# Kernel optimization log

Hardware: AMD Instinct MI355X
Metric: run time of the kernel (lower is better)

The kernel has to match this reference:

```python
import jax, jax.numpy as jnp
import numpy as np

B, S, H = 2, 2048, 2048
E, I, SH = 8, 768, 5632
TOP_K = 2


def setup_inputs() -> dict:
    key = jax.random.key(0)
    ks = jax.random.split(key, 8)
    sc = lambda *shape: 1.0 / np.sqrt(shape[-2] if len(shape) > 1 else 1.0)
    return {
        "hidden_states": jax.random.normal(ks[0], (B, S, H), jnp.float32),
        "router_w": jax.random.normal(ks[1], (H, E), jnp.float32) * (1.0 / np.sqrt(H)),
        "expert_gate_up_w": jax.random.normal(ks[2], (E, H, 2 * I), jnp.float32) * (1.0 / np.sqrt(H)),
        "expert_down_w": jax.random.normal(ks[3], (E, I, H), jnp.float32) * (1.0 / np.sqrt(I)),
        "shared_gate_w": jax.random.normal(ks[4], (H, SH), jnp.float32) * (1.0 / np.sqrt(H)),
        "shared_up_w": jax.random.normal(ks[5], (H, SH), jnp.float32) * (1.0 / np.sqrt(H)),
        "shared_down_w": jax.random.normal(ks[6], (SH, H), jnp.float32) * (1.0 / np.sqrt(SH)),
        "shared_expert_gate_w": jax.random.normal(ks[7], (H, 1), jnp.float32) * (1.0 / np.sqrt(H)),
    }


def reference(hidden_states, router_w, expert_gate_up_w, expert_down_w,
              shared_gate_w, shared_up_w, shared_down_w, shared_expert_gate_w):
    b, s, h = hidden_states.shape
    x = hidden_states.reshape(-1, h)  # [T, H]

    # Shared expert (SwiGLU) gated by sigmoid scalar gate per token.
    gate = jax.nn.silu((x @ shared_gate_w).astype(jnp.float32)).astype(x.dtype)
    shared_out = (gate * (x @ shared_up_w)) @ shared_down_w  # [T, H]
    shared_out = jax.nn.sigmoid(x @ shared_expert_gate_w) * shared_out

    # Router: softmax -> top-k -> renormalize -> dense routing weights [E, T].
    router_logits = x @ router_w  # [T, E]
    router_probs = jax.nn.softmax(router_logits, axis=-1)
    top_p, top_i = jax.lax.top_k(router_probs, TOP_K)  # [T, k]
    top_p = top_p / jnp.sum(top_p, axis=-1, keepdims=True)
    one_hot = jax.nn.one_hot(top_i, E, dtype=top_p.dtype)  # [T, k, E]
    routing_full = jnp.sum(one_hot * top_p[..., None], axis=1)  # [T, E]
    routing_full = routing_full.T.astype(x.dtype)  # [E, T]

    # Dense per-expert SwiGLU over all tokens (as in source einsums).
    gate_up = jnp.einsum('th,ehm->etm', x, expert_gate_up_w)  # [E, T, 2I]
    g, u = jnp.split(gate_up, 2, axis=-1)
    g = jax.nn.silu(g.astype(jnp.float32)).astype(x.dtype)
    expert_out = jnp.einsum('eti,eih->eth', u * g, expert_down_w)  # [E, T, H]

    expert_contribution = jnp.sum(expert_out * routing_full[:, :, None], axis=0)  # [T, H]
    out = (expert_contribution + shared_out).reshape(b, s, h)
    return out, router_logits
```

## Files before the change

### kernel.cpp

```cpp
#include <hip/hip_runtime.h>
#include <hip/hip_bf16.h>
#include <stdint.h>

#define DEVFN static __device__ __forceinline__

typedef __attribute__((ext_vector_type(8))) short bf16x8;
typedef __attribute__((ext_vector_type(4))) float f32x4;
typedef unsigned short u16;
typedef unsigned int u32;
typedef unsigned long long u64;

DEVFN u16 f2bf(float f) {
    union { float f; u32 u; } v; v.f = f;
    u32 r = v.u + 0x7FFFu + ((v.u >> 16) & 1u);
    return (u16)(r >> 16);
}

DEVFN void g2l16(const void* g, void* l) {
    __builtin_amdgcn_global_load_lds(
        (const __attribute__((address_space(1))) u32*)g,
        (__attribute__((address_space(3))) u32*)l, 16, 0, 0);
}

DEVFN void hbar() {
    __asm__ __volatile__("" ::: "memory");
    __builtin_amdgcn_s_barrier();
    __asm__ __volatile__("" ::: "memory");
}
DEVFN void vm4() { asm volatile("s_waitcnt vmcnt(4)" ::: "memory"); }
DEVFN void vm0() { asm volatile("s_waitcnt vmcnt(0)" ::: "memory"); }

#define MFMA16(a, b, c) __builtin_amdgcn_mfma_f32_16x16x32_bf16(a, b, c, 0, 0, 0)

__global__ __launch_bounds__(512, 2) void gemm8_swiglu_k(
    const u16* __restrict__ A, const u16* __restrict__ Bg,
    const u16* __restrict__ Bu, u16* __restrict__ out,
    int K, int nx, int ldc)
{
    extern __shared__ char smraw[];
    char* smA = smraw;
    char* smB = smraw + 65536;

    const int tid = threadIdx.x;
    const int lane = tid & 63, wv = tid >> 6;
    const int wm = wv >> 2, wn = wv & 3;
    const int l15 = lane & 15, kg = lane >> 4;

    const int nwg = gridDim.x;
    const int id = (blockIdx.x & 7) * (nwg >> 3) + (blockIdx.x >> 3);
    const int m0 = (id / nx) * 256, n0 = (id % nx) * 128;

    const u16* Ap  = A  + (long)m0 * K;
    const u16* Bgp = Bg + (long)n0 * K;
    const u16* Bup = Bu + (long)n0 * K;

    f32x4 accg[8][2], accu[8][2];
#pragma unroll
    for (int i = 0; i < 8; ++i)
#pragma unroll
        for (int j = 0; j < 2; ++j) {
            accg[i][j] = f32x4{0.f, 0.f, 0.f, 0.f};
            accu[i][j] = f32x4{0.f, 0.f, 0.f, 0.f};
        }

    auto stA = [&](int kt, int hh, int buf) {
        const u16* src = Ap + ((long)hh * 128) * K + kt * 64;
        char* dst = smA + buf * 32768 + hh * 16384;
#pragma unroll
        for (int i = 0; i < 2; ++i) {
            int slot = i * 512 + tid;
            int row = slot >> 3, ch = slot & 7;
            g2l16(src + (long)row * K + ((ch ^ (row & 7)) << 3), dst + slot * 16);
        }
    };
    auto stB = [&](int kt, int hh, int buf) {
        const u16* src = (hh ? Bup : Bgp) + kt * 64;
        char* dst = smB + buf * 32768 + hh * 16384;
#pragma unroll
        for (int i = 0; i < 2; ++i) {
            int slot = i * 512 + tid;
            int row = slot >> 3, ch = slot & 7;
            g2l16(src + (long)row * K + ((ch ^ (row & 7)) << 3), dst + slot * 16);
        }
    };
    auto frag = [&](const char* base, int r, int c) -> bf16x8 {
        return *(const __attribute__((address_space(3))) bf16x8*)
            (base + r * 128 + (((c) ^ (r & 7)) << 4));
    };

    stA(0, 0, 0); stA(0, 1, 0);
    stB(0, 0, 0); stB(0, 1, 0);
    stB(1, 0, 1); stB(1, 1, 1);
    vm4();
    hbar();

    const int nk = K >> 6;
    for (int kt = 0; kt < nk; kt += 2) {
        const bool more = (kt + 2) < nk;
#pragma unroll
        for (int h = 0; h < 2; ++h) {
            const char* ab = smA + h * 32768;
            const char* bb = smB + h * 32768;
            bf16x8 bgv[2][2], buv[2][2];
#pragma unroll
            for (int p = 0; p < 4; ++p) {
                if (p == 0) {
#pragma unroll
                    for (int fn = 0; fn < 2; ++fn)
#pragma unroll
                        for (int s = 0; s < 2; ++s) {
                            int rB = wn * 32 + fn * 16 + l15;
                            bgv[fn][s] = frag(bb, rB, s * 4 + kg);
                            buv[fn][s] = frag(bb + 16384, rB, s * 4 + kg);
                        }
                }
                bf16x8 av[2][2];
#pragma unroll
                for (int am = 0; am < 2; ++am)
#pragma unroll
                    for (int s = 0; s < 2; ++s)
                        av[am][s] = frag(ab, wm * 128 + (p * 2 + am) * 16 + l15,
                                         s * 4 + kg);
                if (h == 0) {
                    if (p == 0)      { stA(kt + 1, 0, 1); stA(kt + 1, 1, 1); }
                    else if (p == 1) { if (more) stB(kt + 2, 0, 0); }
                    else if (p == 2) { if (more) stB(kt + 2, 1, 0); }
                    else             { if (more) vm4(); else vm0(); }
                } else {
                    if (more) {
                        if (p == 0)      stA(kt + 2, 0, 0);
                        else if (p == 1) stA(kt + 2, 1, 0);
                        else if (p == 2) stB(kt + 3, 0, 1);
                        else             { stB(kt + 3, 1, 1); vm4(); }
                    }
                }
                hbar();
                __builtin_amdgcn_sched_barrier(0);
                __builtin_amdgcn_s_setprio(1);
#pragma unroll
                for (int am = 0; am < 2; ++am)
#pragma unroll
                    for (int s = 0; s < 2; ++s)
#pragma unroll
                        for (int fn = 0; fn < 2; ++fn) {
                            accg[p * 2 + am][fn] = MFMA16(av[am][s], bgv[fn][s],
                                                          accg[p * 2 + am][fn]);
                            accu[p * 2 + am][fn] = MFMA16(av[am][s], buv[fn][s],
                                                          accu[p * 2 + am][fn]);
                        }
                __builtin_amdgcn_s_setprio(0);
                __builtin_amdgcn_sched_barrier(0);
                hbar();
            }
        }
    }

    const int lq = lane >> 4;
#pragma unroll
    for (int fm = 0; fm < 8; ++fm)
#pragma unroll
        for (int j = 0; j < 4; ++j) {
            int row = m0 + wm * 128 + fm * 16 + lq * 4 + j;
#pragma unroll
            for (int fn = 0; fn < 2; ++fn) {
                int col = n0 + wn * 32 + fn * 16 + l15;
                float g = accg[fm][fn][j], u = accu[fm][fn][j];
                float s = g * (1.f / (1.f + __expf(-g))) * u;
                out[(long)row * ldc + col] = f2bf(s);
            }
        }
}

__global__ __launch_bounds__(512, 2) void gemm8e_swiglu_k(
    const u16* __restrict__ xb, const u16* __restrict__ Beg,
    const u16* __restrict__ Beu, const int* __restrict__ tok,
    const int* __restrict__ cntp, u16* __restrict__ eact,
    int K, int ldc, int cap)
{
    const int e = blockIdx.z;
    const int m0 = blockIdx.y * 256;
    if (m0 >= cntp[e]) return;
    const int n0 = blockIdx.x * 128;

    extern __shared__ char smraw[];
    char* smA = smraw;
    char* smB = smraw + 65536;

    const int tid = threadIdx.x;
    const int lane = tid & 63, wv = tid >> 6;
    const int wm = wv >> 2, wn = wv & 3;
    const int l15 = lane & 15, kg = lane >> 4;

    const int r0 = tid >> 3, ch = tid & 7;
    const int swz = (ch ^ (r0 & 7)) << 3;
    const int* tseg = tok + (long)e * cap + m0;
    const u16* pa00 = xb + (long)tseg[r0] * K + swz;
    const u16* pa01 = xb + (long)tseg[64 + r0] * K + swz;
    const u16* pa10 = xb + (long)tseg[128 + r0] * K + swz;
    const u16* pa11 = xb + (long)tseg[192 + r0] * K + swz;

    const u16* Bgp = Beg + ((long)e * ldc + n0) * K;
    const u16* Bup = Beu + ((long)e * ldc + n0) * K;

    f32x4 accg[8][2], accu[8][2];
#pragma unroll
    for (int i = 0; i < 8; ++i)
#pragma unroll
        for (int j = 0; j < 2; ++j) {
            accg[i][j] = f32x4{0.f, 0.f, 0.f, 0.f};
            accu[i][j] = f32x4{0.f, 0.f, 0.f, 0.f};
        }

    auto stA = [&](int kt, int hh, int buf) {
        char* dst = smA + buf * 32768 + hh * 16384;
        const u16* p0 = hh ? pa10 : pa00;
        const u16* p1 = hh ? pa11 : pa01;
        g2l16(p0 + kt * 64, dst + (long)tid * 16);
        g2l16(p1 + kt * 64, dst + (long)(512 + tid) * 16);
    };
    auto stB = [&](int kt, int hh, int buf) {
        const u16* src = (hh ? Bup : Bgp) + kt * 64;
        char* dst = smB + buf * 32768 + hh * 16384;
#pragma unroll
        for (int i = 0; i < 2; ++i) {
            int slot = i * 512 + tid;
            int row = slot >> 3, c = slot & 7;
            g2l16(src + (long)row * K + ((c ^ (row & 7)) << 3), dst + slot * 16);
        }
    };
    auto frag = [&](const char* base, int r, int c) -> bf16x8 {
        return *(const __attribute__((address_space(3))) bf16x8*)
            (base + r * 128 + (((c) ^ (r & 7)) << 4));
    };

    stA(0, 0, 0); stA(0, 1, 0);
    stB(0, 0, 0); stB(0, 1, 0);
    stB(1, 0, 1); stB(1, 1, 1);
    vm4();
    hbar();

    const int nk = K >> 6;
    for (int kt = 0; kt < nk; kt += 2) {
        const bool more = (kt + 2) < nk;
#pragma unroll
        for (int h = 0; h < 2; ++h) {
            const char* ab = smA + h * 32768;
            const char* bb = smB + h * 32768;
            bf16x8 bgv[2][2], buv[2][2];
#pragma unroll
            for (int p = 0; p < 4; ++p) {
                if (p == 0) {
#pragma unroll
                    for (int fn = 0; fn < 2; ++fn)
#pragma unroll
                        for (int s = 0; s < 2; ++s) {
                            int rB = wn * 32 + fn * 16 + l15;
                            bgv[fn][s] = frag(bb, rB, s * 4 + kg);
                            buv[fn][s] = frag(bb + 16384, rB, s * 4 + kg);
                        }
                }
                bf16x8 av[2][2];
#pragma unroll
                for (int am = 0; am < 2; ++am)
#pragma unroll
                    for (int s = 0; s < 2; ++s)
                        av[am][s] = frag(ab, wm * 128 + (p * 2 + am) * 16 + l15,
                                         s * 4 + kg);
                if (h == 0) {
                    if (p == 0)      { stA(kt + 1, 0, 1); stA(kt + 1, 1, 1); }
                    else if (p == 1) { if (more) stB(kt + 2, 0, 0); }
                    else if (p == 2) { if (more) stB(kt + 2, 1, 0); }
                    else             { if (more) vm4(); else vm0(); }
                } else {
                    if (more) {
                        if (p == 0)      stA(kt + 2, 0, 0);
                        else if (p == 1) stA(kt + 2, 1, 0);
                        else if (p == 2) stB(kt + 3, 0, 1);
                        else             { stB(kt + 3, 1, 1); vm4(); }
                    }
                }
                hbar();
                __builtin_amdgcn_sched_barrier(0);
                __builtin_amdgcn_s_setprio(1);
#pragma unroll
                for (int am = 0; am < 2; ++am)
#pragma unroll
                    for (int s = 0; s < 2; ++s)
#pragma unroll
                        for (int fn = 0; fn < 2; ++fn) {
                            accg[p * 2 + am][fn] = MFMA16(av[am][s], bgv[fn][s],
                                                          accg[p * 2 + am][fn]);
                            accu[p * 2 + am][fn] = MFMA16(av[am][s], buv[fn][s],
                                                          accu[p * 2 + am][fn]);
                        }
                __builtin_amdgcn_s_setprio(0);
                __builtin_amdgcn_sched_barrier(0);
                hbar();
            }
        }
    }

    const int lq = lane >> 4;
#pragma unroll
    for (int fm = 0; fm < 8; ++fm)
#pragma unroll
        for (int j = 0; j < 4; ++j) {
            long row = (long)e * cap + m0 + wm * 128 + fm * 16 + lq * 4 + j;
#pragma unroll
            for (int fn = 0; fn < 2; ++fn) {
                int col = n0 + wn * 32 + fn * 16 + l15;
                float g = accg[fm][fn][j], u = accu[fm][fn][j];
                float s = g * (1.f / (1.f + __expf(-g))) * u;
                eact[row * ldc + col] = f2bf(s);
            }
        }
}

template<int NSLOT>
DEVFN void stage(const u16* __restrict__ src, int ldk, u16* lds, int tid) {
#pragma unroll
    for (int i = 0; i < NSLOT / 256; ++i) {
        int slot = i * 256 + tid;
        int row = slot >> 2, chunk = slot & 3;
        int kg = chunk ^ ((row >> 1) & 3);
        g2l16(src + (long)row * ldk + kg * 8, lds + slot * 8);
    }
}

DEVFN bf16x8 ld_frag(const u16* lds, int row, int kg) {
    int chunk = kg ^ ((row >> 1) & 3);
    const u16* p = lds + row * 32 + chunk * 8;
    return *(const __attribute__((address_space(3))) bf16x8*)p;
}

__global__ __launch_bounds__(256) void gemm_down_k(
    const u16* __restrict__ A, const u16* __restrict__ B,
    float* __restrict__ C, const float* __restrict__ gvec,
    int K, int ldc)
{
    __shared__ u16 sm[2][8192];
    const int tid = threadIdx.x;
    const int lane = tid & 63, wv = tid >> 6;
    const int wm = wv >> 1, wn = wv & 1;
    const int m0 = blockIdx.y * 128, n0 = blockIdx.x * 128;
    const u16* Ab = A + (long)m0 * K;
    const u16* Bb = B + (long)n0 * K;

    f32x4 acc[4][4];
#pragma unroll
    for (int i = 0; i < 4; ++i)
#pragma unroll
        for (int j = 0; j < 4; ++j) acc[i][j] = f32x4{0.f, 0.f, 0.f, 0.f};

    stage<512>(Ab, K, &sm[0][0], tid);
    stage<512>(Bb, K, &sm[0][4096], tid);

    const int nk = K >> 5;
    for (int kt = 0; kt < nk; ++kt) {
        const int cur = kt & 1;
        __syncthreads();
        if (kt + 1 < nk) {
            stage<512>(Ab + (kt + 1) * 32, K, &sm[cur ^ 1][0], tid);
            stage<512>(Bb + (kt + 1) * 32, K, &sm[cur ^ 1][4096], tid);
        }
        const int l15 = lane & 15, kg = lane >> 4;
        bf16x8 av[4], bv[4];
#pragma unroll
        for (int f = 0; f < 4; ++f) {
            av[f] = ld_frag(&sm[cur][0],    wm * 64 + f * 16 + l15, kg);
            bv[f] = ld_frag(&sm[cur][4096], wn * 64 + f * 16 + l15, kg);
        }
#pragma unroll
        for (int fm = 0; fm < 4; ++fm)
#pragma unroll
            for (int fn = 0; fn < 4; ++fn)
                acc[fm][fn] = MFMA16(av[fm], bv[fn], acc[fm][fn]);
    }

    const int l15 = lane & 15, lq = lane >> 4;
#pragma unroll
    for (int fm = 0; fm < 4; ++fm) {
#pragma unroll
        for (int j = 0; j < 4; ++j) {
            int row = m0 + wm * 64 + fm * 16 + lq * 4 + j;
            float gmul = gvec[row];
#pragma unroll
            for (int fn = 0; fn < 4; ++fn) {
                int col = n0 + wn * 64 + fn * 16 + l15;
                C[(long)row * ldc + col] = acc[fm][fn][j] * gmul;
            }
        }
    }
}

__global__ __launch_bounds__(256) void gemm_down_moe_k(
    const u16* __restrict__ eact, const u16* __restrict__ Bed,
    float* __restrict__ out, const int* __restrict__ tok,
    const float* __restrict__ wrow, const int* __restrict__ cntp,
    int K, int ldc, int cap)
{
    const int e = blockIdx.z;
    const int m0 = blockIdx.y * 128;
    if (m0 >= cntp[e]) return;
    const int n0 = blockIdx.x * 128;

    __shared__ u16 sm[2][8192];
    const int tid = threadIdx.x;
    const int lane = tid & 63, wv = tid >> 6;
    const int wm = wv >> 1, wn = wv & 1;
    const u16* Ab = eact + ((long)e * cap + m0) * K;
    const u16* Bb = Bed + (long)e * ldc * K + (long)n0 * K;

    f32x4 acc[4][4];
#pragma unroll
    for (int i = 0; i < 4; ++i)
#pragma unroll
        for (int j = 0; j < 4; ++j) acc[i][j] = f32x4{0.f, 0.f, 0.f, 0.f};

    stage<512>(Ab, K, &sm[0][0], tid);
    stage<512>(Bb, K, &sm[0][4096], tid);

    const int nk = K >> 5;
    for (int kt = 0; kt < nk; ++kt) {
        const int cur = kt & 1;
        __syncthreads();
        if (kt + 1 < nk) {
            stage<512>(Ab + (kt + 1) * 32, K, &sm[cur ^ 1][0], tid);
            stage<512>(Bb + (kt + 1) * 32, K, &sm[cur ^ 1][4096], tid);
        }
        const int l15 = lane & 15, kg = lane >> 4;
        bf16x8 av[4], bv[4];
#pragma unroll
        for (int f = 0; f < 4; ++f) {
            av[f] = ld_frag(&sm[cur][0],    wm * 64 + f * 16 + l15, kg);
            bv[f] = ld_frag(&sm[cur][4096], wn * 64 + f * 16 + l15, kg);
        }
#pragma unroll
        for (int fm = 0; fm < 4; ++fm)
#pragma unroll
            for (int fn = 0; fn < 4; ++fn)
                acc[fm][fn] = MFMA16(av[fm], bv[fn], acc[fm][fn]);
    }

    const int l15 = lane & 15, lq = lane >> 4;
#pragma unroll
    for (int fm = 0; fm < 4; ++fm) {
#pragma unroll
        for (int j = 0; j < 4; ++j) {
            long crow = (long)e * cap + m0 + wm * 64 + fm * 16 + lq * 4 + j;
            float w = wrow[crow];
            if (w != 0.f) {
                long t = tok[crow];
#pragma unroll
                for (int fn = 0; fn < 4; ++fn) {
                    int col = n0 + wn * 64 + fn * 16 + l15;
                    atomicAdd(out + t * ldc + col, acc[fm][fn][j] * w);
                }
            }
        }
    }
}

__global__ __launch_bounds__(256) void router_k(
    const float* __restrict__ x, const float* __restrict__ rw,
    const float* __restrict__ sgw, float* __restrict__ logits,
    int2* __restrict__ te, float2* __restrict__ tw,
    float* __restrict__ sig, int T, int H)
{
    const int tid = threadIdx.x, lane = tid & 63, wv = tid >> 6;
    const int t = blockIdx.x * 4 + wv;
    const float* xr = x + (long)t * H;
    float acc[8] = {0, 0, 0, 0, 0, 0, 0, 0};
    float as = 0.f;
    for (int h = lane; h < H; h += 64) {
        float xv = xr[h];
        const float* r = rw + h * 8;
#pragma unroll
        for (int e = 0; e < 8; ++e) acc[e] += xv * r[e];
        as += xv * sgw[h];
    }
#pragma unroll
    for (int off = 32; off; off >>= 1) {
#pragma unroll
        for (int e = 0; e < 8; ++e) acc[e] += __shfl_xor(acc[e], off);
        as += __shfl_xor(as, off);
    }
    if (lane == 0) {
        float mx = acc[0];
#pragma unroll
        for (int e = 1; e < 8; ++e) mx = fmaxf(mx, acc[e]);
        float p[8], sum = 0.f;
#pragma unroll
        for (int e = 0; e < 8; ++e) { p[e] = expf(acc[e] - mx); sum += p[e]; }
        int i1 = 0;
#pragma unroll
        for (int e = 1; e < 8; ++e) if (p[e] > p[i1]) i1 = e;
        int i2 = (i1 == 0) ? 1 : 0;
#pragma unroll
        for (int e = 0; e < 8; ++e) if (e != i1 && p[e] > p[i2]) i2 = e;
        float den = p[i1] + p[i2];
        te[t] = make_int2(i1, i2);
        tw[t] = make_float2(p[i1] / den, p[i2] / den);
#pragma unroll
        for (int e = 0; e < 8; ++e) logits[(long)t * 8 + e] = acc[e];
        sig[t] = 1.f / (1.f + expf(-as));
    }
}

__global__ __launch_bounds__(256) void compact_k(
    const int2* __restrict__ te, const float2* __restrict__ tw,
    int* __restrict__ tok, float* __restrict__ wrow,
    int* __restrict__ cntp, int T, int cap)
{
    const int e = blockIdx.x;
    const int tid = threadIdx.x, lane = tid & 63, wv = tid >> 6;
    __shared__ int wtot[4];
    int cnt = 0;
    for (int c0 = 0; c0 < T; c0 += 256) {
        int t = c0 + tid;
        int2 ids = te[t];
        float2 ws = tw[t];
        float w = (ids.x == e) ? ws.x : ((ids.y == e) ? ws.y : -1.f);
        bool sel = (w >= 0.f);
        u64 b = __ballot(sel);
        int rln = __popcll(b & ((1ull << lane) - 1ull));
        if (lane == 0) wtot[wv] = __popcll(b);
        __syncthreads();
        int rank = rln, tot = 0;
#pragma unroll
        for (int k = 0; k < 4; ++k) { if (k < wv) rank += wtot[k]; tot += wtot[k]; }
        if (sel) {
            int pos = cnt + rank;
            if (pos < cap) {
                tok[(long)e * cap + pos] = t;
                wrow[(long)e * cap + pos] = w;
            }
        }
        cnt += tot;
        __syncthreads();
    }
    if (cnt > cap) cnt = cap;
    int cp = (cnt + 255) & ~255;
    if (cp > cap) cp = cap;
    for (int p = cnt + tid; p < cp; p += 256) {
        tok[(long)e * cap + p] = 0;
        wrow[(long)e * cap + p] = 0.f;
    }
    if (tid == 0) cntp[e] = cp;
}

__global__ __launch_bounds__(256) void transpose_k(
    const float* __restrict__ src0, long src_zstr, int src_ld,
    u16* __restrict__ dst0, long dst_zstr, int dst_ld)
{
    __shared__ float tile[32][33];
    const float* src = src0 + (long)blockIdx.z * src_zstr;
    u16* dst = dst0 + (long)blockIdx.z * dst_zstr;
    int r0 = blockIdx.y * 32, c0 = blockIdx.x * 32;
    int tx = threadIdx.x, ty = threadIdx.y;
#pragma unroll
    for (int k = 0; k < 4; ++k)
        tile[ty + 8 * k][tx] = src[(long)(r0 + ty + 8 * k) * src_ld + c0 + tx];
    __syncthreads();
#pragma unroll
    for (int k = 0; k < 4; ++k)
        dst[(long)(c0 + ty + 8 * k) * dst_ld + r0 + tx] = f2bf(tile[tx][ty + 8 * k]);
}

__global__ __launch_bounds__(256) void cvt_x_k(const float* __restrict__ x,
                                               u16* __restrict__ xb)
{
    long i = ((long)blockIdx.x * 256 + threadIdx.x) * 4;
    float4 v = *(const float4*)(x + i);
    union { u16 s[4]; uint2 v2; } o;
    o.s[0] = f2bf(v.x); o.s[1] = f2bf(v.y); o.s[2] = f2bf(v.z); o.s[3] = f2bf(v.w);
    *(uint2*)(xb + i) = o.v2;
}

extern "C" void kernel_launch(void* const* d_in, const int* in_sizes, int n_in,
                              void* d_out, int out_size, void* d_ws, size_t ws_size,
                              hipStream_t stream) {
    (void)in_sizes; (void)n_in; (void)out_size; (void)ws_size;
    const int Hd = 2048, E = 8, I = 768, SH = 5632, T = 4096, CAP = 2048;

    const float* x    = (const float*)d_in[0];
    const float* rw   = (const float*)d_in[1];
    const float* egu  = (const float*)d_in[2];
    const float* edw  = (const float*)d_in[3];
    const float* sgw  = (const float*)d_in[4];
    const float* suw  = (const float*)d_in[5];
    const float* sdw  = (const float*)d_in[6];
    const float* segw = (const float*)d_in[7];
    float* out = (float*)d_out;
    float* logits = out + (size_t)T * Hd;

    char* wsp = (char*)d_ws;
    size_t off = 0;
    auto alloc = [&](size_t bytes) {
        void* p = wsp + off; off += (bytes + 255) & ~(size_t)255; return p;
    };
    u16* xb   = (u16*)alloc((size_t)T * Hd * 2);
    u16* Bgs  = (u16*)alloc((size_t)SH * Hd * 2);
    u16* Bus  = (u16*)alloc((size_t)SH * Hd * 2);
    u16* Bds  = (u16*)alloc((size_t)Hd * SH * 2);
    u16* Beg  = (u16*)alloc((size_t)E * I * Hd * 2);
    u16* Beu  = (u16*)alloc((size_t)E * I * Hd * 2);
    u16* Bed  = (u16*)alloc((size_t)E * Hd * I * 2);
    u16* hs   = (u16*)alloc((size_t)T * SH * 2);
    u16* eact = (u16*)alloc((size_t)E * CAP * I * 2);
    int2*   te   = (int2*)alloc((size_t)T * 8);
    float2* tw   = (float2*)alloc((size_t)T * 8);
    int*    tok  = (int*)alloc((size_t)E * CAP * 4);
    float*  wrow = (float*)alloc((size_t)E * CAP * 4);
    int*    cntp = (int*)alloc(64);
    float*  sig  = (float*)alloc((size_t)T * 4);

    hipFuncSetAttribute((const void*)gemm8_swiglu_k,
                        hipFuncAttributeMaxDynamicSharedMemorySize, 131072);
    hipFuncSetAttribute((const void*)gemm8e_swiglu_k,
                        hipFuncAttributeMaxDynamicSharedMemorySize, 131072);

    dim3 tb(32, 8);
    cvt_x_k<<<(T * Hd) / 1024, 256, 0, stream>>>(x, xb);
    router_k<<<T / 4, 256, 0, stream>>>(x, rw, segw, logits, te, tw, sig, T, Hd);
    compact_k<<<E, 256, 0, stream>>>(te, tw, tok, wrow, cntp, T, CAP);

    transpose_k<<<dim3(SH / 32, Hd / 32), tb, 0, stream>>>(sgw, 0, SH, Bgs, 0, Hd);
    transpose_k<<<dim3(SH / 32, Hd / 32), tb, 0, stream>>>(suw, 0, SH, Bus, 0, Hd);
    transpose_k<<<dim3(Hd / 32, SH / 32), tb, 0, stream>>>(sdw, 0, Hd, Bds, 0, SH);
    transpose_k<<<dim3(I / 32, Hd / 32, E), tb, 0, stream>>>(
        egu, (long)Hd * 2 * I, 2 * I, Beg, (long)I * Hd, Hd);
    transpose_k<<<dim3(I / 32, Hd / 32, E), tb, 0, stream>>>(
        egu + I, (long)Hd * 2 * I, 2 * I, Beu, (long)I * Hd, Hd);
    transpose_k<<<dim3(Hd / 32, I / 32, E), tb, 0, stream>>>(
        edw, (long)I * Hd, Hd, Bed, (long)Hd * I, I);

    gemm8_swiglu_k<<<dim3((SH / 128) * (T / 256)), 512, 131072, stream>>>(
        xb, Bgs, Bus, hs, Hd, SH / 128, SH);
    gemm_down_k<<<dim3(Hd / 128, T / 128), 256, 0, stream>>>(
        hs, Bds, out, sig, SH, Hd);
    gemm8e_swiglu_k<<<dim3(I / 128, CAP / 256, E), 512, 131072, stream>>>(
        xb, Beg, Beu, tok, cntp, eact, Hd, I, CAP);
    gemm_down_moe_k<<<dim3(Hd / 128, CAP / 128, E), 256, 0, stream>>>(
        eact, Bed, out, tok, wrow, cntp, I, Hd, CAP);
}
```

Measured before the change: 578.6 us.

## Port down-projection GEMMs to 256x256 pipelined kernel with split-K and atomics

Replaces the simple 128x128 double-buffered down-projection kernels (shared and MoE) with the 512-thread 256x256 tile pipeline already used by the gate/up kernels, now wrapped in a shared macro. The shared down GEMM is split along K into two halves that accumulate into a zeroed output with atomics. The B fragments for the next half are also prefetched one phase early to hide LDS latency. This aims to raise MFMA utilisation and data reuse in the down GEMMs, at the cost of an extra memset and atomic traffic on the output.

```diff
diff --git a/kernel.cpp b/kernel.cpp
--- a/kernel.cpp
+++ b/kernel.cpp
@@ -32,6 +32,81 @@
 
 #define MFMA16(a, b, c) __builtin_amdgcn_mfma_f32_16x16x32_bf16(a, b, c, 0, 0, 0)
 
+#define FR(base, r, c) \
+    (*(const __attribute__((address_space(3))) bf16x8*) \
+        ((base) + (r) * 128 + ((((c)) ^ ((r) & 7)) << 4)))
+
+#define RDB8(h) { \
+    const char* _b0 = smB + (h) * 32768; \
+    bgv[h][0][0] = FR(_b0,         wn * 32 +  0 + l15, 0 + kg); \
+    bgv[h][0][1] = FR(_b0,         wn * 32 +  0 + l15, 4 + kg); \
+    bgv[h][1][0] = FR(_b0,         wn * 32 + 16 + l15, 0 + kg); \
+    bgv[h][1][1] = FR(_b0,         wn * 32 + 16 + l15, 4 + kg); \
+    buv[h][0][0] = FR(_b0 + 16384, wn * 32 +  0 + l15, 0 + kg); \
+    buv[h][0][1] = FR(_b0 + 16384, wn * 32 +  0 + l15, 4 + kg); \
+    buv[h][1][0] = FR(_b0 + 16384, wn * 32 + 16 + l15, 0 + kg); \
+    buv[h][1][1] = FR(_b0 + 16384, wn * 32 + 16 + l15, 4 + kg); }
+
+#define PH(h, p, ...) { \
+    const char* _a = smA + (h) * 32768; \
+    bf16x8 a0s0 = FR(_a, wm * 128 + ((p) * 2 + 0) * 16 + l15, 0 + kg); \
+    bf16x8 a0s1 = FR(_a, wm * 128 + ((p) * 2 + 0) * 16 + l15, 4 + kg); \
+    bf16x8 a1s0 = FR(_a, wm * 128 + ((p) * 2 + 1) * 16 + l15, 0 + kg); \
+    bf16x8 a1s1 = FR(_a, wm * 128 + ((p) * 2 + 1) * 16 + l15, 4 + kg); \
+    __VA_ARGS__ \
+    hbar(); \
+    __builtin_amdgcn_sched_barrier(0); \
+    __builtin_amdgcn_s_setprio(1); \
+    accg[(p)*2+0][0] = MFMA16(a0s0, bgv[h][0][0], accg[(p)*2+0][0]); \
+    accu[(p)*2+0][0] = MFMA16(a0s0, buv[h][0][0], accu[(p)*2+0][0]); \
+    accg[(p)*2+0][1] = MFMA16(a0s0, bgv[h][1][0], accg[(p)*2+0][1]); \
+    accu[(p)*2+0][1] = MFMA16(a0s0, buv[h][1][0], accu[(p)*2+0][1]); \
+    accg[(p)*2+0][0] = MFMA16(a0s1, bgv[h][0][1], accg[(p)*2+0][0]); \
+    accu[(p)*2+0][0] = MFMA16(a0s1, buv[h][0][1], accu[(p)*2+0][0]); \
+    accg[(p)*2+0][1] = MFMA16(a0s1, bgv[h][1][1], accg[(p)*2+0][1]); \
+    accu[(p)*2+0][1] = MFMA16(a0s1, buv[h][1][1], accu[(p)*2+0][1]); \
+    accg[(p)*2+1][0] = MFMA16(a1s0, bgv[h][0][0], accg[(p)*2+1][0]); \
+    accu[(p)*2+1][0] = MFMA16(a1s0, buv[h][0][0], accu[(p)*2+1][0]); \
+    accg[(p)*2+1][1] = MFMA16(a1s0, bgv[h][1][0], accg[(p)*2+1][1]); \
+    accu[(p)*2+1][1] = MFMA16(a1s0, buv[h][1][0], accu[(p)*2+1][1]); \
+    accg[(p)*2+1][0] = MFMA16(a1s1, bgv[h][0][1], accg[(p)*2+1][0]); \
+    accu[(p)*2+1][0] = MFMA16(a1s1, buv[h][0][1], accu[(p)*2+1][0]); \
+    accg[(p)*2+1][1] = MFMA16(a1s1, bgv[h][1][1], accg[(p)*2+1][1]); \
+    accu[(p)*2+1][1] = MFMA16(a1s1, buv[h][1][1], accu[(p)*2+1][1]); \
+    __builtin_amdgcn_s_setprio(0); \
+    __builtin_amdgcn_sched_barrier(0); \
+    hbar(); }
+
+#define KLOOP(nk) \
+    stA(0, 0, 0); stA(0, 1, 0); \
+    stB(0, 0, 0); stB(0, 1, 0); \
+    stB(1, 0, 1); stB(1, 1, 1); \
+    vm4(); \
+    hbar(); \
+    RDB8(0); \
+    for (int kt = 0; kt < (nk); kt += 2) { \
+        const bool more = (kt + 2) < (nk); \
+        PH(0, 0, stA(kt + 1, 0, 1); stA(kt + 1, 1, 1); ) \
+        PH(0, 1, if (more) stB(kt + 2, 0, 0); ) \
+        PH(0, 2, if (more) stB(kt + 2, 1, 0); ) \
+        PH(0, 3, if (more) vm4(); else vm0(); RDB8(1); ) \
+        PH(1, 0, if (more) stA(kt + 2, 0, 0); ) \
+        PH(1, 1, if (more) stA(kt + 2, 1, 0); ) \
+        PH(1, 2, if (more) stB(kt + 3, 0, 1); ) \
+        PH(1, 3, if (more) { stB(kt + 3, 1, 1); vm4(); RDB8(0); } ) \
+    }
+
+#define ACC_DECL \
+    f32x4 accg[8][2], accu[8][2]; \
+    _Pragma("unroll") \
+    for (int i = 0; i < 8; ++i) \
+        _Pragma("unroll") \
+        for (int j = 0; j < 2; ++j) { \
+            accg[i][j] = f32x4{0.f, 0.f, 0.f, 0.f}; \
+            accu[i][j] = f32x4{0.f, 0.f, 0.f, 0.f}; \
+        } \
+    bf16x8 bgv[2][2][2], buv[2][2][2];
+
 __global__ __launch_bounds__(512, 2) void gemm8_swiglu_k(
     const u16* __restrict__ A, const u16* __restrict__ Bg,
     const u16* __restrict__ Bu, u16* __restrict__ out,
@@ -54,14 +129,7 @@
     const u16* Bgp = Bg + (long)n0 * K;
     const u16* Bup = Bu + (long)n0 * K;
 
-    f32x4 accg[8][2], accu[8][2];
-#pragma unroll
-    for (int i = 0; i < 8; ++i)
-#pragma unroll
-        for (int j = 0; j < 2; ++j) {
-            accg[i][j] = f32x4{0.f, 0.f, 0.f, 0.f};
-            accu[i][j] = f32x4{0.f, 0.f, 0.f, 0.f};
-        }
+    ACC_DECL;
 
     auto stA = [&](int kt, int hh, int buf) {
         const u16* src = Ap + ((long)hh * 128) * K + kt * 64;
@@ -83,77 +151,8 @@
             g2l16(src + (long)row * K + ((ch ^ (row & 7)) << 3), dst + slot * 16);
         }
     };
-    auto frag = [&](const char* base, int r, int c) -> bf16x8 {
-        return *(const __attribute__((address_space(3))) bf16x8*)
-            (base + r * 128 + (((c) ^ (r & 7)) << 4));
-    };
-
-    stA(0, 0, 0); stA(0, 1, 0);
-    stB(0, 0, 0); stB(0, 1, 0);
-    stB(1, 0, 1); stB(1, 1, 1);
-    vm4();
-    hbar();
-
-    const int nk = K >> 6;
-    for (int kt = 0; kt < nk; kt += 2) {
-        const bool more = (kt + 2) < nk;
-#pragma unroll
-        for (int h = 0; h < 2; ++h) {
-            const char* ab = smA + h * 32768;
-            const char* bb = smB + h * 32768;
-            bf16x8 bgv[2][2], buv[2][2];
-#pragma unroll
-            for (int p = 0; p < 4; ++p) {
-                if (p == 0) {
-#pragma unroll
-                    for (int fn = 0; fn < 2; ++fn)
-#pragma unroll
-                        for (int s = 0; s < 2; ++s) {
-                            int rB = wn * 32 + fn * 16 + l15;
-                            bgv[fn][s] = frag(bb, rB, s * 4 + kg);
-                            buv[fn][s] = frag(bb + 16384, rB, s * 4 + kg);
-                        }
-                }
-                bf16x8 av[2][2];
-#pragma unroll
-                for (int am = 0; am < 2; ++am)
-#pragma unroll
-                    for (int s = 0; s < 2; ++s)
-                        av[am][s] = frag(ab, wm * 128 + (p * 2 + am) * 16 + l15,
-                                         s * 4 + kg);
-                if (h == 0) {
-                    if (p == 0)      { stA(kt + 1, 0, 1); stA(kt + 1, 1, 1); }
-                    else if (p == 1) { if (more) stB(kt + 2, 0, 0); }
-                    else if (p == 2) { if (more) stB(kt + 2, 1, 0); }
-                    else             { if (more) vm4(); else vm0(); }
-                } else {
-                    if (more) {
-                        if (p == 0)      stA(kt + 2, 0, 0);
-                        else if (p == 1) stA(kt + 2, 1, 0);
-                        else if (p == 2) stB(kt + 3, 0, 1);
-                        else             { stB(kt + 3, 1, 1); vm4(); }
-                    }
-                }
-                hbar();
-                __builtin_amdgcn_sched_barrier(0);
-                __builtin_amdgcn_s_setprio(1);
-#pragma unroll
-                for (int am = 0; am < 2; ++am)
-#pragma unroll
-                    for (int s = 0; s < 2; ++s)
-#pragma unroll
-                        for (int fn = 0; fn < 2; ++fn) {
-                            accg[p * 2 + am][fn] = MFMA16(av[am][s], bgv[fn][s],
-                                                          accg[p * 2 + am][fn]);
-                            accu[p * 2 + am][fn] = MFMA16(av[am][s], buv[fn][s],
-                                                          accu[p * 2 + am][fn]);
-                        }
-                __builtin_amdgcn_s_setprio(0);
-                __builtin_amdgcn_sched_barrier(0);
-                hbar();
-            }
-        }
-    }
+
+    KLOOP(K >> 6);
 
     const int lq = lane >> 4;
 #pragma unroll
@@ -202,14 +201,7 @@
     const u16* Bgp = Beg + ((long)e * ldc + n0) * K;
     const u16* Bup = Beu + ((long)e * ldc + n0) * K;
 
-    f32x4 accg[8][2], accu[8][2];
-#pragma unroll
-    for (int i = 0; i < 8; ++i)
-#pragma unroll
-        for (int j = 0; j < 2; ++j) {
-            accg[i][j] = f32x4{0.f, 0.f, 0.f, 0.f};
-            accu[i][j] = f32x4{0.f, 0.f, 0.f, 0.f};
-        }
+    ACC_DECL;
 
     auto stA = [&](int kt, int hh, int buf) {
         char* dst = smA + buf * 32768 + hh * 16384;
@@ -228,77 +220,8 @@
             g2l16(src + (long)row * K + ((c ^ (row & 7)) << 3), dst + slot * 16);
         }
     };
-    auto frag = [&](const char* base, int r, int c) -> bf16x8 {
-        return *(const __attribute__((address_space(3))) bf16x8*)
-            (base + r * 128 + (((c) ^ (r & 7)) << 4));
-    };
-
-    stA(0, 0, 0); stA(0, 1, 0);
-    stB(0, 0, 0); stB(0, 1, 0);
-    stB(1, 0, 1); stB(1, 1, 1);
-    vm4();
-    hbar();
-
-    const int nk = K >> 6;
-    for (int kt = 0; kt < nk; kt += 2) {
-        const bool more = (kt + 2) < nk;
-#pragma unroll
-        for (int h = 0; h < 2; ++h) {
-            const char* ab = smA + h * 32768;
-            const char* bb = smB + h * 32768;
-            bf16x8 bgv[2][2], buv[2][2];
-#pragma unroll
-            for (int p = 0; p < 4; ++p) {
-                if (p == 0) {
-#pragma unroll
-                    for (int fn = 0; fn < 2; ++fn)
-#pragma unroll
-                        for (int s = 0; s < 2; ++s) {
-                            int rB = wn * 32 + fn * 16 + l15;
-                            bgv[fn][s] = frag(bb, rB, s * 4 + kg);
-                            buv[fn][s] = frag(bb + 16384, rB, s * 4 + kg);
-                        }
-                }
-                bf16x8 av[2][2];
-#pragma unroll
-                for (int am = 0; am < 2; ++am)
-#pragma unroll
-                    for (int s = 0; s < 2; ++s)
-                        av[am][s] = frag(ab, wm * 128 + (p * 2 + am) * 16 + l15,
-                                         s * 4 + kg);
-                if (h == 0) {
-                    if (p == 0)      { stA(kt + 1, 0, 1); stA(kt + 1, 1, 1); }
-                    else if (p == 1) { if (more) stB(kt + 2, 0, 0); }
-                    else if (p == 2) { if (more) stB(kt + 2, 1, 0); }
-                    else             { if (more) vm4(); else vm0(); }
-                } else {
-                    if (more) {
-                        if (p == 0)      stA(kt + 2, 0, 0);
-                        else if (p == 1) stA(kt + 2, 1, 0);
-                        else if (p == 2) stB(kt + 3, 0, 1);
-                        else             { stB(kt + 3, 1, 1); vm4(); }
-                    }
-                }
-                hbar();
-                __builtin_amdgcn_sched_barrier(0);
-                __builtin_amdgcn_s_setprio(1);
-#pragma unroll
-                for (int am = 0; am < 2; ++am)
-#pragma unroll
-                    for (int s = 0; s < 2; ++s)
-#pragma unroll
-                        for (int fn = 0; fn < 2; ++fn) {
-                            accg[p * 2 + am][fn] = MFMA16(av[am][s], bgv[fn][s],
-                                                          accg[p * 2 + am][fn]);
-                            accu[p * 2 + am][fn] = MFMA16(av[am][s], buv[fn][s],
-                                                          accu[p * 2 + am][fn]);
-                        }
-                __builtin_amdgcn_s_setprio(0);
-                __builtin_amdgcn_sched_barrier(0);
-                hbar();
-            }
-        }
-    }
+
+    KLOOP(K >> 6);
 
     const int lq = lane >> 4;
 #pragma unroll
@@ -316,149 +239,134 @@
         }
 }
 
-template<int NSLOT>
-DEVFN void stage(const u16* __restrict__ src, int ldk, u16* lds, int tid) {
-#pragma unroll
-    for (int i = 0; i < NSLOT / 256; ++i) {
-        int slot = i * 256 + tid;
-        int row = slot >> 2, chunk = slot & 3;
-        int kg = chunk ^ ((row >> 1) & 3);
-        g2l16(src + (long)row * ldk + kg * 8, lds + slot * 8);
-    }
-}
-
-DEVFN bf16x8 ld_frag(const u16* lds, int row, int kg) {
-    int chunk = kg ^ ((row >> 1) & 3);
-    const u16* p = lds + row * 32 + chunk * 8;
-    return *(const __attribute__((address_space(3))) bf16x8*)p;
-}
-
-__global__ __launch_bounds__(256) void gemm_down_k(
+__global__ __launch_bounds__(512, 2) void gemm8_downks_k(
     const u16* __restrict__ A, const u16* __restrict__ B,
-    float* __restrict__ C, const float* __restrict__ gvec,
-    int K, int ldc)
-{
-    __shared__ u16 sm[2][8192];
+    float* __restrict__ out, const float* __restrict__ sig,
+    int K, int nkh, int ldc)
+{
+    extern __shared__ char smraw[];
+    char* smA = smraw;
+    char* smB = smraw + 65536;
+
     const int tid = threadIdx.x;
     const int lane = tid & 63, wv = tid >> 6;
-    const int wm = wv >> 1, wn = wv & 1;
-    const int m0 = blockIdx.y * 128, n0 = blockIdx.x * 128;
-    const u16* Ab = A + (long)m0 * K;
-    const u16* Bb = B + (long)n0 * K;
-
-    f32x4 acc[4][4];
-#pragma unroll
-    for (int i = 0; i < 4; ++i)
-#pragma unroll
-        for (int j = 0; j < 4; ++j) acc[i][j] = f32x4{0.f, 0.f, 0.f, 0.f};
-
-    stage<512>(Ab, K, &sm[0][0], tid);
-    stage<512>(Bb, K, &sm[0][4096], tid);
-
-    const int nk = K >> 5;
-    for (int kt = 0; kt < nk; ++kt) {
-        const int cur = kt & 1;
-        __syncthreads();
-        if (kt + 1 < nk) {
-            stage<512>(Ab + (kt + 1) * 32, K, &sm[cur ^ 1][0], tid);
-            stage<512>(Bb + (kt + 1) * 32, K, &sm[cur ^ 1][4096], tid);
-        }
-        const int l15 = lane & 15, kg = lane >> 4;
-        bf16x8 av[4], bv[4];
-#pragma unroll
-        for (int f = 0; f < 4; ++f) {
-            av[f] = ld_frag(&sm[cur][0],    wm * 64 + f * 16 + l15, kg);
-            bv[f] = ld_frag(&sm[cur][4096], wn * 64 + f * 16 + l15, kg);
-        }
-#pragma unroll
-        for (int fm = 0; fm < 4; ++fm)
-#pragma unroll
-            for (int fn = 0; fn < 4; ++fn)
-                acc[fm][fn] = MFMA16(av[fm], bv[fn], acc[fm][fn]);
-    }
-
-    const int l15 = lane & 15, lq = lane >> 4;
-#pragma unroll
-    for (int fm = 0; fm < 4; ++fm) {
+    const int wm = wv >> 2, wn = wv & 3;
+    const int l15 = lane & 15, kg = lane >> 4;
+
+    const int m0 = blockIdx.y * 256, n0 = blockIdx.x * 256;
+    const long k0 = (long)blockIdx.z * nkh * 64;
+
+    const u16* Ap  = A + (long)m0 * K + k0;
+    const u16* Blo = B + ((long)(n0      ) * K) + k0;
+    const u16* Bhi = B + ((long)(n0 + 128) * K) + k0;
+
+    ACC_DECL;
+
+    auto stA = [&](int kt, int hh, int buf) {
+        const u16* src = Ap + ((long)hh * 128) * K + kt * 64;
+        char* dst = smA + buf * 32768 + hh * 16384;
+#pragma unroll
+        for (int i = 0; i < 2; ++i) {
+            int slot = i * 512 + tid;
+            int row = slot >> 3, ch = slot & 7;
+            g2l16(src + (long)row * K + ((ch ^ (row & 7)) << 3), dst + slot * 16);
+        }
+    };
+    auto stB = [&](int kt, int hh, int buf) {
+        const u16* src = (hh ? Bhi : Blo) + kt * 64;
+        char* dst = smB + buf * 32768 + hh * 16384;
+#pragma unroll
+        for (int i = 0; i < 2; ++i) {
+            int slot = i * 512 + tid;
+            int row = slot >> 3, ch = slot & 7;
+            g2l16(src + (long)row * K + ((ch ^ (row & 7)) << 3), dst + slot * 16);
+        }
+    };
+
+    KLOOP(nkh);
+
+    const int lq = lane >> 4;
+#pragma unroll
+    for (int fm = 0; fm < 8; ++fm)
 #pragma unroll
         for (int j = 0; j < 4; ++j) {
-            int row = m0 + wm * 64 + fm * 16 + lq * 4 + j;
-            float gmul = gvec[row];
-#pragma unroll
-            for (int fn = 0; fn < 4; ++fn) {
-                int col = n0 + wn * 64 + fn * 16 + l15;
-                C[(long)row * ldc + col] = acc[fm][fn][j] * gmul;
+            int row = m0 + wm * 128 + fm * 16 + lq * 4 + j;
+            float s = sig[row];
+#pragma unroll
+            for (int fn = 0; fn < 2; ++fn) {
+                int col = n0 + wn * 32 + fn * 16 + l15;
+                atomicAdd(out + (long)row * ldc + col, accg[fm][fn][j] * s);
+                atomicAdd(out + (long)row * ldc + col + 128, accu[fm][fn][j] * s);
             }
         }
-    }
-}
-
-__global__ __launch_bounds__(256) void gemm_down_moe_k(
+}
+
+__global__ __launch_bounds__(512, 2) void gemm8_edown_k(
     const u16* __restrict__ eact, const u16* __restrict__ Bed,
     float* __restrict__ out, const int* __restrict__ tok,
     const float* __restrict__ wrow, const int* __restrict__ cntp,
-    int K, int ldc, int cap)
+    int K, int Hd, int cap)
 {
     const int e = blockIdx.z;
-    const int m0 = blockIdx.y * 128;
+    const int m0 = blockIdx.y * 256;
     if (m0 >= cntp[e]) return;
-    const int n0 = blockIdx.x * 128;
-
-    __shared__ u16 sm[2][8192];
+    const int n0 = blockIdx.x * 256;
+
+    extern __shared__ char smraw[];
+    char* smA = smraw;
+    char* smB = smraw + 65536;
+
     const int tid = threadIdx.x;
     const int lane = tid & 63, wv = tid >> 6;
-    const int wm = wv >> 1, wn = wv & 1;
-    const u16* Ab = eact + ((long)e * cap + m0) * K;
-    const u16* Bb = Bed + (long)e * ldc * K + (long)n0 * K;
-
-    f32x4 acc[4][4];
-#pragma unroll
-    for (int i = 0; i < 4; ++i)
-#pragma unroll
-        for (int j = 0; j < 4; ++j) acc[i][j] = f32x4{0.f, 0.f, 0.f, 0.f};
-
-    stage<512>(Ab, K, &sm[0][0], tid);
-    stage<512>(Bb, K, &sm[0][4096], tid);
-
-    const int nk = K >> 5;
-    for (int kt = 0; kt < nk; ++kt) {
-        const int cur = kt & 1;
-        __syncthreads();
-        if (kt + 1 < nk) {
-            stage<512>(Ab + (kt + 1) * 32, K, &sm[cur ^ 1][0], tid);
-            stage<512>(Bb + (kt + 1) * 32, K, &sm[cur ^ 1][4096], tid);
-        }
-        const int l15 = lane & 15, kg = lane >> 4;
-        bf16x8 av[4], bv[4];
-#pragma unroll
-        for (int f = 0; f < 4; ++f) {
-            av[f] = ld_frag(&sm[cur][0],    wm * 64 + f * 16 + l15, kg);
-            bv[f] = ld_frag(&sm[cur][4096], wn * 64 + f * 16 + l15, kg);
-        }
-#pragma unroll
-        for (int fm = 0; fm < 4; ++fm)
-#pragma unroll
-            for (int fn = 0; fn < 4; ++fn)
-                acc[fm][fn] = MFMA16(av[fm], bv[fn], acc[fm][fn]);
-    }
-
-    const int l15 = lane & 15, lq = lane >> 4;
-#pragma unroll
-    for (int fm = 0; fm < 4; ++fm) {
+    const int wm = wv >> 2, wn = wv & 3;
+    const int l15 = lane & 15, kg = lane >> 4;
+
+    const u16* Ap  = eact + ((long)e * cap + m0) * K;
+    const u16* Blo = Bed + ((long)e * Hd + n0      ) * K;
+    const u16* Bhi = Bed + ((long)e * Hd + n0 + 128) * K;
+
+    ACC_DECL;
+
+    auto stA = [&](int kt, int hh, int buf) {
+        const u16* src = Ap + ((long)hh * 128) * K + kt * 64;
+        char* dst = smA + buf * 32768 + hh * 16384;
+#pragma unroll
+        for (int i = 0; i < 2; ++i) {
+            int slot = i * 512 + tid;
+            int row = slot >> 3, ch = slot & 7;
+            g2l16(src + (long)row * K + ((ch ^ (row & 7)) << 3), dst + slot * 16);
+        }
+    };
+    auto stB = [&](int kt, int hh, int buf) {
+        const u16* src = (hh ? Bhi : Blo) + kt * 64;
+        char* dst = smB + buf * 32768 + hh * 16384;
+#pragma unroll
+        for (int i = 0; i < 2; ++i) {
+            int slot = i * 512 + tid;
+            int row = slot >> 3, ch = slot & 7;
+            g2l16(src + (long)row * K + ((ch ^ (row & 7)) << 3), dst + slot * 16);
+        }
+    };
+
+    KLOOP(K >> 6);
+
+    const int lq = lane >> 4;
+#pragma unroll
+    for (int fm = 0; fm < 8; ++fm)
 #pragma unroll
         for (int j = 0; j < 4; ++j) {
-            long crow = (long)e * cap + m0 + wm * 64 + fm * 16 + lq * 4 + j;
+            long crow = (long)e * cap + m0 + wm * 128 + fm * 16 + lq * 4 + j;
             float w = wrow[crow];
             if (w != 0.f) {
                 long t = tok[crow];
 #pragma unroll
-                for (int fn = 0; fn < 4; ++fn) {
-                    int col = n0 + wn * 64 + fn * 16 + l15;
-                    atomicAdd(out + t * ldc + col, acc[fm][fn][j] * w);
+                for (int fn = 0; fn < 2; ++fn) {
+                    int col = n0 + wn * 32 + fn * 16 + l15;
+                    atomicAdd(out + t * Hd + col, accg[fm][fn][j] * w);
+                    atomicAdd(out + t * Hd + col + 128, accu[fm][fn][j] * w);
                 }
             }
         }
-    }
 }
 
 __global__ __launch_bounds__(256) void router_k(
@@ -619,8 +527,13 @@
                         hipFuncAttributeMaxDynamicSharedMemorySize, 131072);
     hipFuncSetAttribute((const void*)gemm8e_swiglu_k,
                         hipFuncAttributeMaxDynamicSharedMemorySize, 131072);
+    hipFuncSetAttribute((const void*)gemm8_downks_k,
+                        hipFuncAttributeMaxDynamicSharedMemorySize, 131072);
+    hipFuncSetAttribute((const void*)gemm8_edown_k,
+                        hipFuncAttributeMaxDynamicSharedMemorySize, 131072);
 
     dim3 tb(32, 8);
+    hipMemsetAsync(out, 0, (size_t)T * Hd * 4, stream);
     cvt_x_k<<<(T * Hd) / 1024, 256, 0, stream>>>(x, xb);
     router_k<<<T / 4, 256, 0, stream>>>(x, rw, segw, logits, te, tw, sig, T, Hd);
     compact_k<<<E, 256, 0, stream>>>(te, tw, tok, wrow, cntp, T, CAP);
@@ -637,10 +550,10 @@
 
     gemm8_swiglu_k<<<dim3((SH / 128) * (T / 256)), 512, 131072, stream>>>(
         xb, Bgs, Bus, hs, Hd, SH / 128, SH);
-    gemm_down_k<<<dim3(Hd / 128, T / 128), 256, 0, stream>>>(
-        hs, Bds, out, sig, SH, Hd);
+    gemm8_downks_k<<<dim3(Hd / 256, T / 256, 2), 512, 131072, stream>>>(
+        hs, Bds, out, sig, SH, (SH / 64) / 2, Hd);
     gemm8e_swiglu_k<<<dim3(I / 128, CAP / 256, E), 512, 131072, stream>>>(
         xb, Beg, Beu, tok, cntp, eact, Hd, I, CAP);
-    gemm_down_moe_k<<<dim3(Hd / 128, CAP / 128, E), 256, 0, stream>>>(
+    gemm8_edown_k<<<dim3(Hd / 256, CAP / 256, E), 512, 131072, stream>>>(
         eact, Bed, out, tok, wrow, cntp, I, Hd, CAP);
 }
```

Result: slower. 805.1 us (+39.1%).

## Replace shared-expert down GEMM with 256x256 split-K pipelined kernel using atomics

Applied to the files above, without the earlier changes.

The simple 128x128 double-buffered shared-expert down-projection GEMM is replaced with a 512-thread kernel that reuses the 8-wave, 256x256-tile pipelined structure of the gate/up kernel. K is split in two across blockIdx.z, and partial results are combined with float atomicAdd into a zeroed output, so a memset is added before the launches. The goal is higher MFMA utilisation, more data reuse per tile, and enough blocks to fill the GPU (16x8x2). The cost is atomic traffic, a non-deterministic summation order, and an extra memset.

```diff
diff --git a/kernel.cpp b/kernel.cpp
--- a/kernel.cpp
+++ b/kernel.cpp
@@ -316,6 +316,144 @@
         }
 }
 
+__global__ __launch_bounds__(512, 2) void gemm8_downks_k(
+    const u16* __restrict__ A, const u16* __restrict__ B,
+    float* __restrict__ out, const float* __restrict__ sig,
+    int K, int nkh, int ldc)
+{
+    extern __shared__ char smraw[];
+    char* smA = smraw;
+    char* smB = smraw + 65536;
+
+    const int tid = threadIdx.x;
+    const int lane = tid & 63, wv = tid >> 6;
+    const int wm = wv >> 2, wn = wv & 3;
+    const int l15 = lane & 15, kg = lane >> 4;
+
+    const int m0 = blockIdx.y * 256, n0 = blockIdx.x * 256;
+    const long k0 = (long)blockIdx.z * nkh * 64;
+
+    const u16* Ap  = A + (long)m0 * K + k0;
+    const u16* Blo = B + (long)n0 * K + k0;
+    const u16* Bhi = B + (long)(n0 + 128) * K + k0;
+
+    f32x4 accg[8][2], accu[8][2];
+#pragma unroll
+    for (int i = 0; i < 8; ++i)
+#pragma unroll
+        for (int j = 0; j < 2; ++j) {
+            accg[i][j] = f32x4{0.f, 0.f, 0.f, 0.f};
+            accu[i][j] = f32x4{0.f, 0.f, 0.f, 0.f};
+        }
+
+    auto stA = [&](int kt, int hh, int buf) {
+        const u16* src = Ap + ((long)hh * 128) * K + kt * 64;
+        char* dst = smA + buf * 32768 + hh * 16384;
+#pragma unroll
+        for (int i = 0; i < 2; ++i) {
+            int slot = i * 512 + tid;
+            int row = slot >> 3, ch = slot & 7;
+            g2l16(src + (long)row * K + ((ch ^ (row & 7)) << 3), dst + slot * 16);
+        }
+    };
+    auto stB = [&](int kt, int hh, int buf) {
+        const u16* src = (hh ? Bhi : Blo) + kt * 64;
+        char* dst = smB + buf * 32768 + hh * 16384;
+#pragma unroll
+        for (int i = 0; i < 2; ++i) {
+            int slot = i * 512 + tid;
+            int row = slot >> 3, ch = slot & 7;
+            g2l16(src + (long)row * K + ((ch ^ (row & 7)) << 3), dst + slot * 16);
+        }
+    };
+    auto frag = [&](const char* base, int r, int c) -> bf16x8 {
+        return *(const __attribute__((address_space(3))) bf16x8*)
+            (base + r * 128 + (((c) ^ (r & 7)) << 4));
+    };
+
+    stA(0, 0, 0); stA(0, 1, 0);
+    stB(0, 0, 0); stB(0, 1, 0);
+    stB(1, 0, 1); stB(1, 1, 1);
+    vm4();
+    hbar();
+
+    const int nk = nkh;
+    for (int kt = 0; kt < nk; kt += 2) {
+        const bool more = (kt + 2) < nk;
+#pragma unroll
+        for (int h = 0; h < 2; ++h) {
+            const char* ab = smA + h * 32768;
+            const char* bb = smB + h * 32768;
+            bf16x8 bgv[2][2], buv[2][2];
+#pragma unroll
+            for (int p = 0; p < 4; ++p) {
+                if (p == 0) {
+#pragma unroll
+                    for (int fn = 0; fn < 2; ++fn)
+#pragma unroll
+                        for (int s = 0; s < 2; ++s) {
+                            int rB = wn * 32 + fn * 16 + l15;
+                            bgv[fn][s] = frag(bb, rB, s * 4 + kg);
+                            buv[fn][s] = frag(bb + 16384, rB, s * 4 + kg);
+                        }
+                }
+                bf16x8 av[2][2];
+#pragma unroll
+                for (int am = 0; am < 2; ++am)
+#pragma unroll
+                    for (int s = 0; s < 2; ++s)
+                        av[am][s] = frag(ab, wm * 128 + (p * 2 + am) * 16 + l15,
+                                         s * 4 + kg);
+                if (h == 0) {
+                    if (p == 0)      { stA(kt + 1, 0, 1); stA(kt + 1, 1, 1); }
+                    else if (p == 1) { if (more) stB(kt + 2, 0, 0); }
+                    else if (p == 2) { if (more) stB(kt + 2, 1, 0); }
+                    else             { if (more) vm4(); else vm0(); }
+                } else {
+                    if (more) {
+                        if (p == 0)      stA(kt + 2, 0, 0);
+                        else if (p == 1) stA(kt + 2, 1, 0);
+                        else if (p == 2) stB(kt + 3, 0, 1);
+                        else             { stB(kt + 3, 1, 1); vm4(); }
+                    }
+                }
+                hbar();
+                __builtin_amdgcn_sched_barrier(0);
+                __builtin_amdgcn_s_setprio(1);
+#pragma unroll
+                for (int am = 0; am < 2; ++am)
+#pragma unroll
+                    for (int s = 0; s < 2; ++s)
+#pragma unroll
+                        for (int fn = 0; fn < 2; ++fn) {
+                            accg[p * 2 + am][fn] = MFMA16(av[am][s], bgv[fn][s],
+                                                          accg[p * 2 + am][fn]);
+                            accu[p * 2 + am][fn] = MFMA16(av[am][s], buv[fn][s],
+                                                          accu[p * 2 + am][fn]);
+                        }
+                __builtin_amdgcn_s_setprio(0);
+                __builtin_amdgcn_sched_barrier(0);
+                hbar();
+            }
+        }
+    }
+
+    const int lq = lane >> 4;
+#pragma unroll
+    for (int fm = 0; fm < 8; ++fm)
+#pragma unroll
+        for (int j = 0; j < 4; ++j) {
+            int row = m0 + wm * 128 + fm * 16 + lq * 4 + j;
+            float s = sig[row];
+#pragma unroll
+            for (int fn = 0; fn < 2; ++fn) {
+                int col = n0 + wn * 32 + fn * 16 + l15;
+                atomicAdd(out + (long)row * ldc + col, accg[fm][fn][j] * s);
+                atomicAdd(out + (long)row * ldc + col + 128, accu[fm][fn][j] * s);
+            }
+        }
+}
+
 template<int NSLOT>
 DEVFN void stage(const u16* __restrict__ src, int ldk, u16* lds, int tid) {
 #pragma unroll
@@ -331,66 +469,6 @@
     int chunk = kg ^ ((row >> 1) & 3);
     const u16* p = lds + row * 32 + chunk * 8;
     return *(const __attribute__((address_space(3))) bf16x8*)p;
-}
-
-__global__ __launch_bounds__(256) void gemm_down_k(
-    const u16* __restrict__ A, const u16* __restrict__ B,
-    float* __restrict__ C, const float* __restrict__ gvec,
-    int K, int ldc)
-{
-    __shared__ u16 sm[2][8192];
-    const int tid = threadIdx.x;
-    const int lane = tid & 63, wv = tid >> 6;
-    const int wm = wv >> 1, wn = wv & 1;
-    const int m0 = blockIdx.y * 128, n0 = blockIdx.x * 128;
-    const u16* Ab = A + (long)m0 * K;
-    const u16* Bb = B + (long)n0 * K;
-
-    f32x4 acc[4][4];
-#pragma unroll
-    for (int i = 0; i < 4; ++i)
-#pragma unroll
-        for (int j = 0; j < 4; ++j) acc[i][j] = f32x4{0.f, 0.f, 0.f, 0.f};
-
-    stage<512>(Ab, K, &sm[0][0], tid);
-    stage<512>(Bb, K, &sm[0][4096], tid);
-
-    const int nk = K >> 5;
-    for (int kt = 0; kt < nk; ++kt) {
-        const int cur = kt & 1;
-        __syncthreads();
-        if (kt + 1 < nk) {
-            stage<512>(Ab + (kt + 1) * 32, K, &sm[cur ^ 1][0], tid);
-            stage<512>(Bb + (kt + 1) * 32, K, &sm[cur ^ 1][4096], tid);
-        }
-        const int l15 = lane & 15, kg = lane >> 4;
-        bf16x8 av[4], bv[4];
-#pragma unroll
-        for (int f = 0; f < 4; ++f) {
-            av[f] = ld_frag(&sm[cur][0],    wm * 64 + f * 16 + l15, kg);
-            bv[f] = ld_frag(&sm[cur][4096], wn * 64 + f * 16 + l15, kg);
-        }
-#pragma unroll
-        for (int fm = 0; fm < 4; ++fm)
-#pragma unroll
-            for (int fn = 0; fn < 4; ++fn)
-                acc[fm][fn] = MFMA16(av[fm], bv[fn], acc[fm][fn]);
-    }
-
-    const int l15 = lane & 15, lq = lane >> 4;
-#pragma unroll
-    for (int fm = 0; fm < 4; ++fm) {
-#pragma unroll
-        for (int j = 0; j < 4; ++j) {
-            int row = m0 + wm * 64 + fm * 16 + lq * 4 + j;
-            float gmul = gvec[row];
-#pragma unroll
-            for (int fn = 0; fn < 4; ++fn) {
-                int col = n0 + wn * 64 + fn * 16 + l15;
-                C[(long)row * ldc + col] = acc[fm][fn][j] * gmul;
-            }
-        }
-    }
 }
 
 __global__ __launch_bounds__(256) void gemm_down_moe_k(
@@ -619,8 +697,11 @@
                         hipFuncAttributeMaxDynamicSharedMemorySize, 131072);
     hipFuncSetAttribute((const void*)gemm8e_swiglu_k,
                         hipFuncAttributeMaxDynamicSharedMemorySize, 131072);
+    hipFuncSetAttribute((const void*)gemm8_downks_k,
+                        hipFuncAttributeMaxDynamicSharedMemorySize, 131072);
 
     dim3 tb(32, 8);
+    hipMemsetAsync(out, 0, (size_t)T * Hd * 4, stream);
     cvt_x_k<<<(T * Hd) / 1024, 256, 0, stream>>>(x, xb);
     router_k<<<T / 4, 256, 0, stream>>>(x, rw, segw, logits, te, tw, sig, T, Hd);
     compact_k<<<E, 256, 0, stream>>>(te, tw, tok, wrow, cntp, T, CAP);
@@ -637,8 +718,8 @@
 
     gemm8_swiglu_k<<<dim3((SH / 128) * (T / 256)), 512, 131072, stream>>>(
         xb, Bgs, Bus, hs, Hd, SH / 128, SH);
-    gemm_down_k<<<dim3(Hd / 128, T / 128), 256, 0, stream>>>(
-        hs, Bds, out, sig, SH, Hd);
+    gemm8_downks_k<<<dim3(Hd / 256, T / 256, 2), 512, 131072, stream>>>(
+        hs, Bds, out, sig, SH, (SH / 64) / 2, Hd);
     gemm8e_swiglu_k<<<dim3(I / 128, CAP / 256, E), 512, 131072, stream>>>(
         xb, Beg, Beu, tok, cntp, eact, Hd, I, CAP);
     gemm_down_moe_k<<<dim3(Hd / 128, CAP / 128, E), 256, 0, stream>>>(
```

Measured after the change: 603.2 us. +4.3%, slower.
